# Performance work log

Hardware: AMD Instinct MI355X
Metric: run time of the kernel (lower is better)

Reference implementation:

```python
import jax, jax.numpy as jnp
import numpy as np

B, S, L = 8, 512, 1536          # batch, new tokens, cached tokens
H, HQ, HKV, D = 4096, 32, 8, 128
THETA = 500000.0


def _rope(x, pos):
    # x: [b, s, h, d]; pos: [s] absolute positions. Llama half-split RoPE.
    half = D // 2
    inv_freq = 1.0 / (THETA ** (jnp.arange(half, dtype=jnp.float32) / half))
    ang = pos.astype(jnp.float32)[:, None] * inv_freq[None, :]      # [s, half]
    cos = jnp.cos(ang)[None, :, None, :]
    sin = jnp.sin(ang)[None, :, None, :]
    x1, x2 = x[..., :half], x[..., half:]
    return jnp.concatenate([x1 * cos - x2 * sin, x2 * cos + x1 * sin], axis=-1)


def setup_inputs() -> dict:
    key = jax.random.key(0)
    ks = jax.random.split(key, 7)
    return {
        "hidden_states": jax.random.normal(ks[0], (B, S, H), jnp.float32),
        "k_cache": jax.random.normal(ks[1], (B, L, HKV, D), jnp.float32),
        "v_cache": jax.random.normal(ks[2], (B, L, HKV, D), jnp.float32),
        "wq": jax.random.normal(ks[3], (H, HQ * D), jnp.float32) * (H ** -0.5),
        "wk": jax.random.normal(ks[4], (H, HKV * D), jnp.float32) * (H ** -0.5),
        "wv": jax.random.normal(ks[5], (H, HKV * D), jnp.float32) * (H ** -0.5),
        "wo": jax.random.normal(ks[6], (HQ * D, H), jnp.float32) * ((HQ * D) ** -0.5),
    }


def reference(hidden_states, k_cache, v_cache, wq, wk, wv, wo):
    b, s, _ = hidden_states.shape
    # fused QKV projections (bias=False)
    q = (hidden_states @ wq).reshape(b, s, HQ, D)
    k = (hidden_states @ wk).reshape(b, s, HKV, D)
    v = (hidden_states @ wv).reshape(b, s, HKV, D)

    pos = L + jnp.arange(s)                     # absolute positions of new tokens
    q = _rope(q, pos)
    k = _rope(k, pos)

    # append new tokens to the (already-rotated) KV cache
    K = jnp.concatenate([k_cache, k], axis=1)   # [b, T, hkv, d]
    V = jnp.concatenate([v_cache, v], axis=1)
    T = K.shape[1]

    g = HQ // HKV                               # GQA group size
    qg = q.reshape(b, s, HKV, g, D)
    scores = jnp.einsum("bskgd,btkd->bskgt", qg, K) * (D ** -0.5)

    # causal mask: query at global position L+i attends to kv position t <= L+i
    allowed = jnp.arange(T)[None, :] <= (L + jnp.arange(s))[:, None]   # [s, T]
    scores = jnp.where(allowed[None, :, None, None, :], scores, jnp.finfo(scores.dtype).min)

    attn = jax.nn.softmax(scores, axis=-1)
    out = jnp.einsum("bskgt,btkd->bskgd", attn, V).reshape(b, s, HQ * D)
    return out @ wo
```

## Files before the change

kernel.cpp:

```cpp
#include <hip/hip_runtime.h>
#include <cstdint>
#include <cstddef>

#define B_   8
#define S_   512
#define L_   1536
#define T_   2048
#define H_   4096
#define HQ_  32
#define HKV_ 8
#define D_   128

typedef __bf16 bf16;
typedef __bf16 bf16x8 __attribute__((ext_vector_type(8)));
typedef float  f32x4  __attribute__((ext_vector_type(4)));

#define LOG2_THETA 18.931568569324174f
#define SCL (0.08838834764831845f * 1.4426950408889634f)

__device__ __forceinline__ void gld_lds16(const void* g, void* l) {
    __builtin_amdgcn_global_load_lds(
        (const __attribute__((address_space(1))) void*)g,
        (__attribute__((address_space(3))) void*)l, 16, 0, 0);
}

__global__ void pack_bf16(const float* __restrict__ src, bf16* __restrict__ dst, int n4) {
    int i = blockIdx.x * 256 + threadIdx.x;
    if (i >= n4) return;
    float4 v = ((const float4*)src)[i];
    bf16 h[4] = {(bf16)v.x, (bf16)v.y, (bf16)v.z, (bf16)v.w};
    *(uint2*)(dst + 4 * (size_t)i) = *(const uint2*)h;
}

__global__ void transpose_pack(const float* __restrict__ src, bf16* __restrict__ dst,
                               int N, int rowOff) {
    __shared__ float t[32][33];
    int n0 = blockIdx.x * 32, k0 = blockIdx.y * 32;
    int c = threadIdx.x & 31, r = threadIdx.x >> 5;
    for (int i = 0; i < 4; i++)
        t[r + 8 * i][c] = src[(size_t)(k0 + r + 8 * i) * N + n0 + c];
    __syncthreads();
    for (int i = 0; i < 4; i++)
        dst[(size_t)(rowOff + n0 + r + 8 * i) * 4096 + k0 + c] = (bf16)t[c][r + 8 * i];
}

template <bool OUT_BF16>
__global__ __launch_bounds__(256) void gemm128(const bf16* __restrict__ A,
                                               const bf16* __restrict__ Bt,
                                               void* __restrict__ Cv,
                                               int M, int N, int K) {
    __shared__ alignas(16) bf16 As[128 * 64];
    __shared__ alignas(16) bf16 Bs[128 * 64];
    int tid = threadIdx.x, lane = tid & 63, wid = tid >> 6;
    int l15 = lane & 15, q4 = lane >> 4;
    int m0 = blockIdx.y * 128, n0 = blockIdx.x * 128;
    int wm = (wid >> 1) * 64, wn = (wid & 1) * 64;

    f32x4 acc[4][4];
    for (int i = 0; i < 4; i++)
        for (int j = 0; j < 4; j++)
            acc[i][j] = (f32x4){0.f, 0.f, 0.f, 0.f};

    for (int k0 = 0; k0 < K; k0 += 64) {
        for (int r = 0; r < 4; ++r) {
            int i = r * 256 + tid;
            int row = i >> 3, c = i & 7;
            int sc = c ^ (row & 7);
            int ldsBase = (i & ~63) * 8;
            gld_lds16(A + (size_t)(m0 + row) * K + k0 + sc * 8, &As[ldsBase]);
            gld_lds16(Bt + (size_t)(n0 + row) * K + k0 + sc * 8, &Bs[ldsBase]);
        }
        __syncthreads();
        for (int kc = 0; kc < 2; ++kc) {
            bf16x8 af[4], bfr[4];
            for (int mi = 0; mi < 4; mi++) {
                int m = wm + mi * 16 + l15;
                int c = (kc * 4 + q4) ^ (m & 7);
                af[mi] = *(const bf16x8*)&As[m * 64 + c * 8];
            }
            for (int ni = 0; ni < 4; ni++) {
                int n = wn + ni * 16 + l15;
                int c = (kc * 4 + q4) ^ (n & 7);
                bfr[ni] = *(const bf16x8*)&Bs[n * 64 + c * 8];
            }
            for (int mi = 0; mi < 4; mi++)
                for (int ni = 0; ni < 4; ni++)
                    acc[mi][ni] = __builtin_amdgcn_mfma_f32_16x16x32_bf16(
                        af[mi], bfr[ni], acc[mi][ni], 0, 0, 0);
        }
        __syncthreads();
    }
    int col0 = n0 + wn + l15;
    int rbase = m0 + wm + q4 * 4;
    for (int mi = 0; mi < 4; mi++)
        for (int ni = 0; ni < 4; ni++)
            for (int r = 0; r < 4; r++) {
                size_t row = rbase + mi * 16 + r;
                size_t col = col0 + ni * 16;
                if (OUT_BF16)
                    ((bf16*)Cv)[row * N + col] = (bf16)acc[mi][ni][r];
                else
                    ((float*)Cv)[row * N + col] = acc[mi][ni][r];
            }
}

__device__ __forceinline__ float rope_val(const bf16* row, int d, int pos) {
    int i = d & 63;
    float inv = exp2f(-(float)i * (LOG2_THETA / 64.0f));
    float ang = (float)pos * inv;
    float sn, cs;
    sincosf(ang, &sn, &cs);
    float x = (float)row[d];
    float xo = (float)row[(d < 64) ? d + 64 : d - 64];
    return (d < 64) ? x * cs - xo * sn : x * cs + xo * sn;
}

__global__ void rope_q(const bf16* __restrict__ qkv, bf16* __restrict__ Qb) {
    size_t idx = (size_t)blockIdx.x * 256 + threadIdx.x;
    int d = idx & 127;
    int h = (idx >> 7) & 31;
    int m = idx >> 12;
    int s = m & 511;
    const bf16* row = qkv + (size_t)m * 6144 + h * 128;
    Qb[idx] = (bf16)(rope_val(row, d, L_ + s) * SCL);
}

__global__ void build_k(const bf16* __restrict__ qkv, const float* __restrict__ kcache,
                        bf16* __restrict__ Kf) {
    size_t idx = (size_t)blockIdx.x * 256 + threadIdx.x;
    int d = idx & 127;
    int hk = (idx >> 7) & 7;
    int t = (idx >> 10) & 2047;
    int b = idx >> 21;
    if (t < L_) {
        Kf[idx] = (bf16)kcache[(((size_t)b * L_ + t) * HKV_ + hk) * D_ + d];
    } else {
        int s = t - L_;
        const bf16* row = qkv + (size_t)(b * S_ + s) * 6144 + 4096 + hk * 128;
        Kf[idx] = (bf16)rope_val(row, d, t);
    }
}

__global__ void build_vT(const bf16* __restrict__ qkv, const float* __restrict__ vcache,
                         bf16* __restrict__ VtG) {
    __shared__ float tile[32][33];
    int t0 = blockIdx.x * 32, d0 = blockIdx.y * 32, z = blockIdx.z;
    int b = z >> 3, hk = z & 7;
    int c = threadIdx.x & 31, r = threadIdx.x >> 5;
    if (t0 < L_) {
        for (int i = 0; i < 4; i++)
            tile[r + 8 * i][c] =
                vcache[(((size_t)b * L_ + t0 + r + 8 * i) * HKV_ + hk) * D_ + d0 + c];
    } else {
        for (int i = 0; i < 4; i++)
            tile[r + 8 * i][c] =
                (float)qkv[(size_t)(b * S_ + t0 - L_ + r + 8 * i) * 6144 + 5120 + hk * 128 + d0 + c];
    }
    __syncthreads();
    for (int i = 0; i < 4; i++)
        VtG[((size_t)(b * 8 + hk) * 128 + d0 + r + 8 * i) * T_ + t0 + c] = (bf16)tile[c][r + 8 * i];
}

__global__ __launch_bounds__(256) void attn(const bf16* __restrict__ Q,
                                            const bf16* __restrict__ Kf,
                                            const bf16* __restrict__ VtG,
                                            bf16* __restrict__ Ao) {
    __shared__ alignas(16) bf16 Kl[64 * 128];
    __shared__ alignas(16) bf16 Vl[128 * 64];
    __shared__ alignas(16) bf16 Pl[4 * 32 * 64];

    int tid = threadIdx.x, lane = tid & 63, w = tid >> 6;
    int l15 = lane & 15, q4 = lane >> 4;
    int bid = blockIdx.x;
    int b = bid & 7, hk = (bid >> 3) & 7, scb = bid >> 6;
    int s0 = scb * 32;
    int sbw = s0 + w * 8;
    int swz = l15 & 7;

    bf16x8 qf[2][4];
    for (int mt = 0; mt < 2; mt++) {
        int s_q = sbw + mt * 4 + (l15 >> 2);
        int h = hk * 4 + (l15 & 3);
        const bf16* qp = Q + (((size_t)(b * S_ + s_q) * HQ_ + h) << 7);
        for (int kc = 0; kc < 4; kc++) qf[mt][kc] = *(const bf16x8*)(qp + kc * 32 + q4 * 8);
    }

    f32x4 O[2][8];
    float lsum[2][4];
    for (int mt = 0; mt < 2; mt++) {
        for (int dt = 0; dt < 8; dt++) O[mt][dt] = (f32x4){0.f, 0.f, 0.f, 0.f};
        for (int r = 0; r < 4; r++) lsum[mt][r] = 0.f;
    }

    int ntiles = (L_ + s0 + 32 + 63) >> 6;
    const bf16* Kbase = Kf + ((size_t)b * T_ * HKV_ + hk) * D_;
    const bf16* Vbase = VtG + (size_t)(b * 8 + hk) * 128 * T_;

    for (int tile = 0; tile < ntiles; ++tile) {
        int t0 = tile << 6;
        for (int it = 0; it < 4; it++) {
            int ci = it * 256 + tid;
            int key = ci >> 4, c = ci & 15, sc = c ^ (key & 7);
            gld_lds16(Kbase + (size_t)(t0 + key) * (HKV_ * D_) + sc * 8, &Kl[(ci & ~63) * 8]);
        }
        for (int it = 0; it < 4; it++) {
            int ci = it * 256 + tid;
            int row = ci >> 3, c = ci & 7, sc = c ^ (row & 7);
            gld_lds16(Vbase + (size_t)row * T_ + t0 + sc * 8, &Vl[(ci & ~63) * 8]);
        }
        __syncthreads();

        if (t0 <= L_ + sbw + 7) {
            f32x4 sv[2][4];
            for (int mt = 0; mt < 2; mt++)
                for (int kg = 0; kg < 4; kg++) sv[mt][kg] = (f32x4){0.f, 0.f, 0.f, 0.f};
            for (int kg = 0; kg < 4; kg++) {
                bf16x8 kfr[4];
                int krow = kg * 16 + l15;
                for (int kc = 0; kc < 4; kc++)
                    kfr[kc] = *(const bf16x8*)&Kl[krow * 128 + (((kc * 4 + q4) ^ swz) * 8)];
                for (int mt = 0; mt < 2; mt++)
                    for (int kc = 0; kc < 4; kc++)
                        sv[mt][kg] = __builtin_amdgcn_mfma_f32_16x16x32_bf16(
                            qf[mt][kc], kfr[kc], sv[mt][kg], 0, 0, 0);
            }
            bool need_mask = (t0 + 63 > L_ + sbw);
            for (int mt = 0; mt < 2; mt++) {
                int lim = L_ + sbw + mt * 4 + q4;
                for (int kg = 0; kg < 4; kg++) {
                    int tK = t0 + kg * 16 + l15;
                    for (int r = 0; r < 4; r++) {
                        float z = sv[mt][kg][r];
                        if (need_mask && tK > lim) z = -3.0e38f;
                        z = __builtin_amdgcn_exp2f(z);
                        lsum[mt][r] += z;
                        int rr = mt * 16 + q4 * 4 + r;
                        int cpos = (kg * 2 + (l15 >> 3)) ^ (rr & 7);
                        Pl[w * 2048 + rr * 64 + cpos * 8 + (l15 & 7)] = (bf16)z;
                    }
                }
            }
            for (int kcv = 0; kcv < 2; kcv++) {
                bf16x8 pf[2];
                for (int mt = 0; mt < 2; mt++)
                    pf[mt] = *(const bf16x8*)&Pl[w * 2048 + (mt * 16 + l15) * 64 +
                                                 (((kcv * 4 + q4) ^ swz) * 8)];
                for (int dt = 0; dt < 8; dt++) {
                    bf16x8 vfr = *(const bf16x8*)&Vl[(dt * 16 + l15) * 64 +
                                                     (((kcv * 4 + q4) ^ swz) * 8)];
                    for (int mt = 0; mt < 2; mt++)
                        O[mt][dt] = __builtin_amdgcn_mfma_f32_16x16x32_bf16(
                            pf[mt], vfr, O[mt][dt], 0, 0, 0);
                }
            }
        }
        __syncthreads();
    }

    for (int mt = 0; mt < 2; mt++)
        for (int r = 0; r < 4; r++) {
            float v = lsum[mt][r];
            for (int off = 1; off < 16; off <<= 1) v += __shfl_xor(v, off, 16);
            lsum[mt][r] = 1.f / v;
        }
    for (int mt = 0; mt < 2; mt++) {
        int s = sbw + mt * 4 + q4;
        for (int r = 0; r < 4; r++) {
            size_t base = (((size_t)(b * S_ + s) * HQ_ + hk * 4 + r) << 7);
            for (int dt = 0; dt < 8; dt++)
                Ao[base + dt * 16 + l15] = (bf16)(O[mt][dt][r] * lsum[mt][r]);
        }
    }
}

extern "C" void kernel_launch(void* const* d_in, const int* in_sizes, int n_in,
                              void* d_out, int out_size, void* d_ws, size_t ws_size,
                              hipStream_t stream) {
    const float* hs = (const float*)d_in[0];
    const float* kc = (const float*)d_in[1];
    const float* vc = (const float*)d_in[2];
    const float* wq = (const float*)d_in[3];
    const float* wk = (const float*)d_in[4];
    const float* wv = (const float*)d_in[5];
    const float* wo = (const float*)d_in[6];
    float* out = (float*)d_out;
    char* ws = (char*)d_ws;

    const size_t SZ_HB   = (size_t)4096 * 4096 * 2;
    const size_t SZ_WQKV = (size_t)6144 * 4096 * 2;
    const size_t SZ_WO   = (size_t)4096 * 4096 * 2;
    const size_t SZ_QKV  = (size_t)4096 * 6144 * 2;
    const size_t SZ_Q    = (size_t)4096 * 4096 * 2;
    const size_t SZ_KV   = (size_t)B_ * T_ * HKV_ * D_ * 2;

    bf16* hb    = (bf16*)(ws);
    bf16* wqkvt = (bf16*)(ws + SZ_HB);
    bf16* wot   = (bf16*)(ws + SZ_HB + SZ_WQKV);
    bf16* qkv   = (bf16*)(ws + SZ_HB + SZ_WQKV + SZ_WO);
    bf16* qb    = (bf16*)(ws + SZ_HB + SZ_WQKV + SZ_WO + SZ_QKV);
    bf16* kf    = (bf16*)(ws + SZ_HB + SZ_WQKV + SZ_WO + SZ_QKV + SZ_Q);
    bf16* vtg   = (bf16*)(ws + SZ_HB + SZ_WQKV + SZ_WO + SZ_QKV + SZ_Q + SZ_KV);
    bf16* ao    = hb;

    pack_bf16<<<16384, 256, 0, stream>>>(hs, hb, 4096 * 4096 / 4);
    transpose_pack<<<dim3(128, 128), 256, 0, stream>>>(wq, wqkvt, 4096, 0);
    transpose_pack<<<dim3(32, 128), 256, 0, stream>>>(wk, wqkvt, 1024, 4096);
    transpose_pack<<<dim3(32, 128), 256, 0, stream>>>(wv, wqkvt, 1024, 5120);
    transpose_pack<<<dim3(128, 128), 256, 0, stream>>>(wo, wot, 4096, 0);
    gemm128<true><<<dim3(48, 32), 256, 0, stream>>>(hb, wqkvt, qkv, 4096, 6144, 4096);
    rope_q<<<65536, 256, 0, stream>>>(qkv, qb);
    build_k<<<65536, 256, 0, stream>>>(qkv, kc, kf);
    build_vT<<<dim3(64, 4, 64), 256, 0, stream>>>(qkv, vc, vtg);
    attn<<<1024, 256, 0, stream>>>(qb, kf, vtg, ao);
    gemm128<false><<<dim3(32, 32), 256, 0, stream>>>(ao, wot, out, 4096, 4096, 4096);
}
```

Before: 1.012 ms.

## Replace 128x128 GEMM with double-buffered 256x256 tile, 8-wave pipelined kernel

Replaces the single-buffered 128x128 GEMM with a 256x256 tile, 512-thread kernel. It double-buffers LDS, interleaves global-to-LDS loads with MFMA phases, and raises priority around the MFMA blocks. The larger tiles are meant to raise arithmetic intensity, and the overlap is meant to hide load latency behind compute for both projection GEMMs. In exchange it uses 128KB of LDS and far fewer blocks: 384 and 256 against 256 CUs, which risks wave-quantization tail effects. The waitcnt bookkeeping is hand-tuned and fragile.

```diff
diff --git a/kernel.cpp b/kernel.cpp
--- a/kernel.cpp
+++ b/kernel.cpp
@@ -23,6 +23,13 @@
         (const __attribute__((address_space(1))) void*)g,
         (__attribute__((address_space(3))) void*)l, 16, 0, 0);
 }
+
+#define BAR()                                   \
+    do {                                        \
+        asm volatile("" ::: "memory");          \
+        __builtin_amdgcn_s_barrier();           \
+        asm volatile("" ::: "memory");          \
+    } while (0)
 
 __global__ void pack_bf16(const float* __restrict__ src, bf16* __restrict__ dst, int n4) {
     int i = blockIdx.x * 256 + threadIdx.x;
@@ -45,63 +52,121 @@
 }
 
 template <bool OUT_BF16>
-__global__ __launch_bounds__(256) void gemm128(const bf16* __restrict__ A,
-                                               const bf16* __restrict__ Bt,
-                                               void* __restrict__ Cv,
-                                               int M, int N, int K) {
-    __shared__ alignas(16) bf16 As[128 * 64];
-    __shared__ alignas(16) bf16 Bs[128 * 64];
-    int tid = threadIdx.x, lane = tid & 63, wid = tid >> 6;
-    int l15 = lane & 15, q4 = lane >> 4;
-    int m0 = blockIdx.y * 128, n0 = blockIdx.x * 128;
-    int wm = (wid >> 1) * 64, wn = (wid & 1) * 64;
-
-    f32x4 acc[4][4];
-    for (int i = 0; i < 4; i++)
-        for (int j = 0; j < 4; j++)
-            acc[i][j] = (f32x4){0.f, 0.f, 0.f, 0.f};
-
-    for (int k0 = 0; k0 < K; k0 += 64) {
-        for (int r = 0; r < 4; ++r) {
-            int i = r * 256 + tid;
-            int row = i >> 3, c = i & 7;
-            int sc = c ^ (row & 7);
-            int ldsBase = (i & ~63) * 8;
-            gld_lds16(A + (size_t)(m0 + row) * K + k0 + sc * 8, &As[ldsBase]);
-            gld_lds16(Bt + (size_t)(n0 + row) * K + k0 + sc * 8, &Bs[ldsBase]);
-        }
-        __syncthreads();
-        for (int kc = 0; kc < 2; ++kc) {
-            bf16x8 af[4], bfr[4];
-            for (int mi = 0; mi < 4; mi++) {
-                int m = wm + mi * 16 + l15;
-                int c = (kc * 4 + q4) ^ (m & 7);
-                af[mi] = *(const bf16x8*)&As[m * 64 + c * 8];
-            }
-            for (int ni = 0; ni < 4; ni++) {
-                int n = wn + ni * 16 + l15;
-                int c = (kc * 4 + q4) ^ (n & 7);
-                bfr[ni] = *(const bf16x8*)&Bs[n * 64 + c * 8];
-            }
-            for (int mi = 0; mi < 4; mi++)
-                for (int ni = 0; ni < 4; ni++)
-                    acc[mi][ni] = __builtin_amdgcn_mfma_f32_16x16x32_bf16(
-                        af[mi], bfr[ni], acc[mi][ni], 0, 0, 0);
-        }
-        __syncthreads();
-    }
-    int col0 = n0 + wn + l15;
-    int rbase = m0 + wm + q4 * 4;
-    for (int mi = 0; mi < 4; mi++)
-        for (int ni = 0; ni < 4; ni++)
-            for (int r = 0; r < 4; r++) {
-                size_t row = rbase + mi * 16 + r;
-                size_t col = col0 + ni * 16;
+__global__ __launch_bounds__(512, 2) void gemm256(const bf16* __restrict__ A,
+                                                  const bf16* __restrict__ Bt,
+                                                  void* __restrict__ Cv,
+                                                  int M, int N, int K) {
+    __shared__ alignas(16) bf16 As[2][256 * 64];
+    __shared__ alignas(16) bf16 Bs[2][256 * 64];
+
+    const int tid = threadIdx.x, lane = tid & 63;
+    const int wid = tid >> 6, wm = wid >> 2, wn = wid & 3;
+    const int l15 = lane & 15, q4 = lane >> 4;
+
+    const int m0 = blockIdx.y * 256, n0 = blockIdx.x * 256;
+    const int nkt = K >> 6;
+    const int NITER = K >> 7;
+
+    const int scs = (((tid & 7) ^ ((tid >> 3) & 7)) * 8);
+    const size_t offg0 = (size_t)(tid >> 3) * K + scs;
+    const size_t offg1 = offg0 + (size_t)64 * K;
+    const int lds0 = (tid & ~63) * 8;
+    const int lds1 = lds0 + 4096;
+
+    const bf16* Ag = A + (size_t)m0 * K;
+    const bf16* Bg = Bt + (size_t)n0 * K;
+
+    const int swz = l15 & 7;
+    const int cc0 = ((0 + q4) ^ swz) * 8;
+    const int cc1 = ((4 + q4) ^ swz) * 8;
+
+#define ST(G, ARR, BUF, H, KT)                                                \
+    if ((KT) < nkt) {                                                         \
+        gld_lds16(G + (size_t)(H) * 128 * K + (size_t)(KT) * 64 + offg0,      \
+                  &ARR[BUF][(H) * 8192 + lds0]);                              \
+        gld_lds16(G + (size_t)(H) * 128 * K + (size_t)(KT) * 64 + offg1,      \
+                  &ARR[BUF][(H) * 8192 + lds1]);                              \
+    }
+
+#define RDA(BUF, MH)                                                           \
+    _Pragma("unroll") for (int mi = 0; mi < 4; ++mi) {                         \
+        const bf16* p = &As[BUF][(wm * 128 + (MH) * 64 + mi * 16 + l15) * 64]; \
+        afr[mi][0] = *(const bf16x8*)(p + cc0);                                \
+        afr[mi][1] = *(const bf16x8*)(p + cc1);                                \
+    }
+
+#define RDB(BUF, NH)                                                           \
+    _Pragma("unroll") for (int ni = 0; ni < 2; ++ni) {                         \
+        const bf16* p = &Bs[BUF][(wn * 64 + (NH) * 32 + ni * 16 + l15) * 64];  \
+        bfr[NH][ni][0] = *(const bf16x8*)(p + cc0);                            \
+        bfr[NH][ni][1] = *(const bf16x8*)(p + cc1);                            \
+    }
+
+#define MM(MH, NH)                                                             \
+    __builtin_amdgcn_s_setprio(1);                                             \
+    _Pragma("unroll") for (int mi = 0; mi < 4; ++mi)                           \
+    _Pragma("unroll") for (int ni = 0; ni < 2; ++ni) {                         \
+        acc[(MH)*4 + mi][(NH)*2 + ni] = __builtin_amdgcn_mfma_f32_16x16x32_bf16( \
+            afr[mi][0], bfr[NH][ni][0], acc[(MH)*4 + mi][(NH)*2 + ni], 0, 0, 0); \
+        acc[(MH)*4 + mi][(NH)*2 + ni] = __builtin_amdgcn_mfma_f32_16x16x32_bf16( \
+            afr[mi][1], bfr[NH][ni][1], acc[(MH)*4 + mi][(NH)*2 + ni], 0, 0, 0); \
+    }                                                                          \
+    __builtin_amdgcn_s_setprio(0);
+
+    f32x4 acc[8][4];
+#pragma unroll
+    for (int i = 0; i < 8; ++i)
+#pragma unroll
+        for (int j = 0; j < 4; ++j) acc[i][j] = (f32x4){0.f, 0.f, 0.f, 0.f};
+
+    bf16x8 afr[4][2];
+    bf16x8 bfr[2][2][2];
+
+    ST(Bg, Bs, 0, 0, 0); ST(Bg, Bs, 0, 1, 0);
+    ST(Ag, As, 0, 0, 0); ST(Ag, As, 0, 1, 0);
+    ST(Bg, Bs, 1, 0, 1); ST(Bg, Bs, 1, 1, 1);
+    asm volatile("s_waitcnt vmcnt(4)" ::: "memory");
+    BAR();
+
+    for (int it = 0; it < NITER; ++it) {
+        const int t1 = 2 * it + 1, t2 = 2 * it + 2, t3 = 2 * it + 3;
+        RDA(0, 0); RDB(0, 0); ST(Ag, As, 1, 0, t1); BAR(); MM(0, 0); BAR();
+        RDB(0, 1);            ST(Ag, As, 1, 1, t1); BAR(); MM(0, 1); BAR();
+        RDA(0, 1);            ST(Bg, Bs, 0, 0, t2); BAR(); MM(1, 0); BAR();
+                              ST(Bg, Bs, 0, 1, t2); BAR(); MM(1, 1);
+        if (it == NITER - 1) {
+            asm volatile("s_waitcnt vmcnt(0)" ::: "memory");
+        } else {
+            asm volatile("s_waitcnt vmcnt(4)" ::: "memory");
+        }
+        BAR();
+        RDA(1, 0); RDB(1, 0); ST(Ag, As, 0, 0, t2); BAR(); MM(0, 0); BAR();
+        RDB(1, 1);            ST(Ag, As, 0, 1, t2); BAR(); MM(0, 1); BAR();
+        RDA(1, 1);            ST(Bg, Bs, 1, 0, t3); BAR(); MM(1, 0); BAR();
+                              ST(Bg, Bs, 1, 1, t3); BAR(); MM(1, 1);
+        asm volatile("s_waitcnt vmcnt(4)" ::: "memory");
+        BAR();
+    }
+
+    const int colb = n0 + wn * 64 + l15;
+    const int rowb = m0 + wm * 128 + q4 * 4;
+#pragma unroll
+    for (int mi = 0; mi < 8; ++mi)
+#pragma unroll
+        for (int ni = 0; ni < 4; ++ni)
+#pragma unroll
+            for (int r = 0; r < 4; ++r) {
+                size_t row = (size_t)(rowb + mi * 16 + r);
+                size_t col = (size_t)(colb + ni * 16);
                 if (OUT_BF16)
                     ((bf16*)Cv)[row * N + col] = (bf16)acc[mi][ni][r];
                 else
                     ((float*)Cv)[row * N + col] = acc[mi][ni][r];
             }
+#undef ST
+#undef RDA
+#undef RDB
+#undef MM
 }
 
 __device__ __forceinline__ float rope_val(const bf16* row, int d, int pos) {
@@ -307,10 +372,10 @@
     transpose_pack<<<dim3(32, 128), 256, 0, stream>>>(wk, wqkvt, 1024, 4096);
     transpose_pack<<<dim3(32, 128), 256, 0, stream>>>(wv, wqkvt, 1024, 5120);
     transpose_pack<<<dim3(128, 128), 256, 0, stream>>>(wo, wot, 4096, 0);
-    gemm128<true><<<dim3(48, 32), 256, 0, stream>>>(hb, wqkvt, qkv, 4096, 6144, 4096);
+    gemm256<true><<<dim3(24, 16), 512, 0, stream>>>(hb, wqkvt, qkv, 4096, 6144, 4096);
     rope_q<<<65536, 256, 0, stream>>>(qkv, qb);
     build_k<<<65536, 256, 0, stream>>>(qkv, kc, kf);
     build_vT<<<dim3(64, 4, 64), 256, 0, stream>>>(qkv, vc, vtg);
     attn<<<1024, 256, 0, stream>>>(qb, kf, vtg, ao);
-    gemm128<false><<<dim3(32, 32), 256, 0, stream>>>(ao, wot, out, 4096, 4096, 4096);
-}
+    gemm256<false><<<dim3(16, 16), 512, 0, stream>>>(ao, wot, out, 4096, 4096, 4096);
+}
```

Measured after the change: 987.3 us. 2.5% less time.
